# Optimization experiments

Hardware: AMD Instinct MI355X
Metric: run time of the kernel (lower is better)

The kernel has to match this reference:

```python
import jax, jax.numpy as jnp
import numpy as np

DIM = 1024
NUM_HEAD = 16
N_IMG = 64


def _linear_params(key, scale=0.02):
    kw, kb = jax.random.split(key)
    W = jax.random.normal(kw, (DIM, DIM), jnp.float32) * scale
    b = jax.random.normal(kb, (DIM,), jnp.float32) * scale
    return W, b


def setup_inputs() -> dict:
    key = jax.random.key(0)
    ks = jax.random.split(key, 5)
    # ragged per-image instance counts: 128..254, deterministic, sum = 12224
    lens = (128 + 2 * np.arange(N_IMG)).astype(np.int64)
    N = int(lens.sum())  # 12224
    x = jax.random.normal(ks[0], (N, DIM), jnp.float32)
    Wq, bq = _linear_params(ks[1])
    Wk, bk = _linear_params(ks[2])
    Wv, bv = _linear_params(ks[3])
    Wu, bu = _linear_params(ks[4])
    return {"x": x, "Wq": Wq, "bq": bq, "Wk": Wk, "bk": bk,
            "Wv": Wv, "bv": bv, "Wu": Wu, "bu": bu,
            "num_inst_per_image": jnp.asarray(lens)}


def _segment_layout(num_inst_per_image):
    # static (int) metadata -> numpy; returns padded gather idx, key mask, unpad idx
    lens = np.asarray(num_inst_per_image)
    B = lens.shape[0]
    L = int(lens.max())
    offsets = np.concatenate([[0], np.cumsum(lens)[:-1]])
    pos = offsets[:, None] + np.arange(L)[None, :]           # [B, L] flat positions
    valid = np.arange(L)[None, :] < lens[:, None]            # [B, L]
    gather_idx = jnp.asarray(np.where(valid, pos, 0))        # safe gather
    flat_take = jnp.asarray(np.flatnonzero(valid.ravel()))   # [N] unpad (row-major = segment order)
    return gather_idx, jnp.asarray(valid), flat_take, B, L


def reference(x, Wq, bq, Wk, bk, Wv, bv, Wu, bu, num_inst_per_image):
    gather_idx, valid, flat_take, B, L = _segment_layout(num_inst_per_image)
    N, C = x.shape
    H = NUM_HEAD
    D = C // H
    # global QKV projections on the flat batch (as in the torch module)
    q = (x @ Wq + bq)[gather_idx].reshape(B, L, H, D)
    k = (x @ Wk + bk)[gather_idx].reshape(B, L, H, D)
    v = (x @ Wv + bv)[gather_idx].reshape(B, L, H, D)
    scale = 1.0 / np.sqrt(C)  # note: original divides by sqrt(C), not sqrt(head_dim)
    attn = jnp.einsum('bqhd,bkhd->bhqk', q, k) * scale       # [B, H, L, L]
    bias = jnp.where(valid[:, None, None, :], 0.0, -jnp.inf)  # mask padded keys
    attn = jax.nn.softmax(attn + bias, axis=-1)
    out = jnp.einsum('bhqk,bkhd->bqhd', attn, v).reshape(B * L, C)
    out = out[flat_take]                                      # unpad back to [N, C]
    return out @ Wu + bu
```

## Files before the change

### kernel.cpp

```cpp
#include <hip/hip_runtime.h>
#include <hip/hip_bf16.h>
#include <math.h>

#define DIMC 1024
#define NHEAD 16
#define HDIM 64
#define MPAD 12288

using bf16x8 = __attribute__((ext_vector_type(8))) short;
using f32x4  = __attribute__((ext_vector_type(4))) float;
using f32x16 = __attribute__((ext_vector_type(16))) float;

__device__ inline ushort f2bf(float f) {
    uint u = __float_as_uint(f);
    u += 0x7fffu + ((u >> 16) & 1u);
    return (ushort)(u >> 16);
}
__device__ inline float bf2f(ushort h) { return __uint_as_float(((uint)h) << 16); }

__device__ inline uint pkbf(float a, float b) {
    __hip_bfloat162 t = __float22bfloat162_rn(float2{a, b});
    return *reinterpret_cast<uint*>(&t);
}

__device__ inline void gload_lds16(const ushort* g, ushort* l) {
    __builtin_amdgcn_global_load_lds(
        (const __attribute__((address_space(1))) uint*)g,
        (__attribute__((address_space(3))) uint*)l, 16, 0, 0);
}

__global__ __launch_bounds__(256) void gemm_qkv(
    const ushort* __restrict__ A, const ushort* __restrict__ Bt,
    const float* __restrict__ bq, const float* __restrict__ bk,
    const float* __restrict__ bv,
    ushort* __restrict__ qb, ushort* __restrict__ kb, ushort* __restrict__ vb,
    int M)
{
    __shared__ ushort As[128 * 32];
    __shared__ ushort Bs[128 * 32];

    const int bid = blockIdx.x;
    const int xcd = bid & 7;
    const int j   = bid >> 3;
    const int mt  = xcd * 12 + (j % 12);
    const int nt  = j / 12;
    const int row0 = mt * 128, col0 = nt * 128;

    const int t    = threadIdx.x;
    const int w    = t >> 6;
    const int lane = t & 63;
    const int wr   = (w >> 1) * 64;
    const int wc   = (w & 1) * 64;
    const int frow = lane & 15;
    const int fk   = (lane >> 4) * 8;
    const int arow = lane >> 2;
    const int acol = (lane & 3) * 8;

    f32x4 acc[4][4] = {};

    for (int k0 = 0; k0 < DIMC; k0 += 32) {
        #pragma unroll
        for (int i = 0; i < 2; ++i) {
            const int rr = (i * 4 + w) * 16;
            gload_lds16(A  + (size_t)(row0 + rr + arow) * DIMC + k0 + acol, As + rr * 32);
            gload_lds16(Bt + (size_t)(col0 + rr + arow) * DIMC + k0 + acol, Bs + rr * 32);
        }
        __syncthreads();

        bf16x8 af[4], bfr[4];
        #pragma unroll
        for (int m = 0; m < 4; ++m)
            af[m]  = *(const bf16x8*)&As[(wr + m * 16 + frow) * 32 + fk];
        #pragma unroll
        for (int n = 0; n < 4; ++n)
            bfr[n] = *(const bf16x8*)&Bs[(wc + n * 16 + frow) * 32 + fk];

        #pragma unroll
        for (int m = 0; m < 4; ++m)
            #pragma unroll
            for (int n = 0; n < 4; ++n)
                acc[m][n] = __builtin_amdgcn_mfma_f32_16x16x32_bf16(
                    af[m], bfr[n], acc[m][n], 0, 0, 0);
        __syncthreads();
    }

    const int sel = nt >> 3;
    const float* bias = (sel == 0) ? bq : (sel == 1) ? bk : bv;
    ushort* outp      = (sel == 0) ? qb : (sel == 1) ? kb : vb;
    const int colb = col0 - sel * 1024;

    const int r4 = (lane >> 4) * 4;
    #pragma unroll
    for (int n = 0; n < 4; ++n) {
        const int c  = colb + wc + n * 16 + (lane & 15);
        const float bb = bias[c];
        #pragma unroll
        for (int m = 0; m < 4; ++m) {
            #pragma unroll
            for (int r = 0; r < 4; ++r) {
                const int gr = row0 + wr + m * 16 + r4 + r;
                if (gr < M)
                    outp[(size_t)gr * DIMC + c] = f2bf(acc[m][n][r] + bb);
            }
        }
    }
}

__global__ __launch_bounds__(256) void gemm_final(
    const ushort* __restrict__ A, const ushort* __restrict__ Bt,
    const float* __restrict__ bias, float* __restrict__ C, int M)
{
    __shared__ ushort As[128 * 32];
    __shared__ ushort Bs[128 * 32];

    const int bid = blockIdx.x;
    const int xcd = bid & 7;
    const int j   = bid >> 3;
    const int mt  = xcd * 12 + (j % 12);
    const int nt  = j / 12;
    const int row0 = mt * 128, col0 = nt * 128;

    const int t    = threadIdx.x;
    const int w    = t >> 6;
    const int lane = t & 63;
    const int wr   = (w >> 1) * 64;
    const int wc   = (w & 1) * 64;
    const int frow = lane & 15;
    const int fk   = (lane >> 4) * 8;
    const int arow = lane >> 2;
    const int acol = (lane & 3) * 8;

    f32x4 acc[4][4] = {};

    for (int k0 = 0; k0 < DIMC; k0 += 32) {
        #pragma unroll
        for (int i = 0; i < 2; ++i) {
            const int rr = (i * 4 + w) * 16;
            gload_lds16(A  + (size_t)(row0 + rr + arow) * DIMC + k0 + acol, As + rr * 32);
            gload_lds16(Bt + (size_t)(col0 + rr + arow) * DIMC + k0 + acol, Bs + rr * 32);
        }
        __syncthreads();

        bf16x8 af[4], bfr[4];
        #pragma unroll
        for (int m = 0; m < 4; ++m)
            af[m]  = *(const bf16x8*)&As[(wr + m * 16 + frow) * 32 + fk];
        #pragma unroll
        for (int n = 0; n < 4; ++n)
            bfr[n] = *(const bf16x8*)&Bs[(wc + n * 16 + frow) * 32 + fk];

        #pragma unroll
        for (int m = 0; m < 4; ++m)
            #pragma unroll
            for (int n = 0; n < 4; ++n)
                acc[m][n] = __builtin_amdgcn_mfma_f32_16x16x32_bf16(
                    af[m], bfr[n], acc[m][n], 0, 0, 0);
        __syncthreads();
    }

    const int r4 = (lane >> 4) * 4;
    #pragma unroll
    for (int n = 0; n < 4; ++n) {
        const int c  = col0 + wc + n * 16 + (lane & 15);
        const float bb = bias[c];
        #pragma unroll
        for (int m = 0; m < 4; ++m) {
            #pragma unroll
            for (int r = 0; r < 4; ++r) {
                const int gr = row0 + wr + m * 16 + r4 + r;
                if (gr < M)
                    C[(size_t)gr * DIMC + c] = acc[m][n][r] + bb;
            }
        }
    }
}

__global__ __launch_bounds__(256) void cvt_pad(
    const float* __restrict__ x, ushort* __restrict__ xb, int nvalid, int ntot)
{
    const int stride = gridDim.x * blockDim.x;
    for (int i = blockIdx.x * blockDim.x + threadIdx.x; i < ntot / 4; i += stride) {
        const int e = i * 4;
        ushort4 o;
        if (e < nvalid) {
            const float4 f = *(const float4*)(x + e);
            o.x = f2bf(f.x); o.y = f2bf(f.y); o.z = f2bf(f.z); o.w = f2bf(f.w);
        } else { o.x = o.y = o.z = o.w = 0; }
        *(ushort4*)(xb + e) = o;
    }
}

__global__ __launch_bounds__(256) void transpose_w4(
    const float* __restrict__ W0, const float* __restrict__ W1,
    const float* __restrict__ W2, const float* __restrict__ W3,
    ushort* __restrict__ T0, ushort* __restrict__ T1,
    ushort* __restrict__ T2, ushort* __restrict__ T3)
{
    __shared__ float tile[32][33];
    const int z = blockIdx.z;
    const float* W = (z == 0) ? W0 : (z == 1) ? W1 : (z == 2) ? W2 : W3;
    ushort*      T = (z == 0) ? T0 : (z == 1) ? T1 : (z == 2) ? T2 : T3;
    const int tx = threadIdx.x & 31;
    const int ty = threadIdx.x >> 5;
    const int n0 = blockIdx.x * 32;
    const int k0 = blockIdx.y * 32;
    #pragma unroll
    for (int i = 0; i < 32; i += 8)
        tile[ty + i][tx] = W[(size_t)(k0 + ty + i) * DIMC + n0 + tx];
    __syncthreads();
    #pragma unroll
    for (int i = 0; i < 32; i += 8)
        T[(size_t)(n0 + ty + i) * DIMC + k0 + tx] = f2bf(tile[tx][ty + i]);
}

__global__ __launch_bounds__(64) void attn_mfma(
    const ushort* __restrict__ qg, const ushort* __restrict__ kg,
    const ushort* __restrict__ vg, ushort* __restrict__ og,
    const int* __restrict__ lens, int B)
{
    __shared__ ushort Vt[64 * 68];

    const int i   = blockIdx.x;
    const int xcd = i & 7;
    const int j   = i >> 3;
    const int bh  = xcd * (B * 2) + (j >> 2);
    const int qt  = j & 3;
    const int h   = bh & 15;
    const int b   = bh >> 4;

    const int lane = threadIdx.x & 63;

    const int myl = (lane < B) ? lens[lane] : 0;
    int inc = myl;
    #pragma unroll
    for (int d = 1; d < 64; d <<= 1) {
        const int nb = __shfl_up(inc, d);
        if (lane >= d) inc += nb;
    }
    const int off = __shfl(inc, b) - __shfl(myl, b);
    const int L   = __shfl(myl, b);
    if (qt * 64 >= L) return;
    const int ntk = (L + 63) >> 6;

    const int l31 = lane & 31;
    const int hi  = lane >> 5;
    const int kp  = lane & 31;
    const int dh  = lane >> 5;

    bf16x8 qf[2][4];
    #pragma unroll
    for (int qn = 0; qn < 2; ++qn) {
        const size_t row = (size_t)(off + min(qt * 64 + qn * 32 + l31, L - 1));
        #pragma unroll
        for (int ks = 0; ks < 4; ++ks) {
            union { uint4 u4; ushort us[8]; bf16x8 v; } tmp;
            tmp.u4 = *(const uint4*)(qg + row * DIMC + h * HDIM + ks * 16 + hi * 8);
            #pragma unroll
            for (int e = 0; e < 8; ++e)
                tmp.us[e] = f2bf(bf2f(tmp.us[e]) * 0.03125f);
            qf[qn][ks] = tmp.v;
        }
    }

    f32x16 o[2][2] = {};
    float mst[2] = {-1e30f, -1e30f};
    float lst[2] = {0.f, 0.f};

    uint4 va[4], vbr[4];
    auto issueV = [&](int tt) {
        const int j0s = tt * 64;
        #pragma unroll
        for (int it = 0; it < 4; ++it) {
            const int d0 = (it * 2 + dh) * 8;
            const size_t r0 = (size_t)(off + min(j0s + 2 * kp,     L - 1));
            const size_t r1 = (size_t)(off + min(j0s + 2 * kp + 1, L - 1));
            va[it]  = *(const uint4*)(vg + r0 * DIMC + h * HDIM + d0);
            vbr[it] = *(const uint4*)(vg + r1 * DIMC + h * HDIM + d0);
        }
    };

    bf16x8 kfc[2][4], kfn[2][4];
    auto loadK = [&](int tt, bf16x8 (&kf)[2][4]) {
        const int j0s = tt * 64;
        #pragma unroll
        for (int km = 0; km < 2; ++km) {
            const size_t row = (size_t)(off + min(j0s + km * 32 + l31, L - 1));
            #pragma unroll
            for (int ks = 0; ks < 4; ++ks)
                kf[km][ks] = *(const bf16x8*)(kg + row * DIMC + h * HDIM + ks * 16 + hi * 8);
        }
    };

    issueV(0);
    loadK(0, kfc);

    for (int t = 0; t < ntk; ++t) {
        const int j0 = t * 64;

        loadK(min(t + 1, ntk - 1), kfn);

        f32x16 s[2][2] = {};
        __builtin_amdgcn_s_setprio(1);
        #pragma unroll
        for (int km = 0; km < 2; ++km)
            #pragma unroll
            for (int qn = 0; qn < 2; ++qn)
                #pragma unroll
                for (int ks = 0; ks < 4; ++ks)
                    s[km][qn] = __builtin_amdgcn_mfma_f32_32x32x16_bf16(
                        kfc[km][ks], qf[qn][ks], s[km][qn], 0, 0, 0);
        __builtin_amdgcn_s_setprio(0);

        #pragma unroll
        for (int it = 0; it < 4; ++it) {
            const int d0 = (it * 2 + dh) * 8;
            const uint a4[4] = {va[it].x,  va[it].y,  va[it].z,  va[it].w};
            const uint b4[4] = {vbr[it].x, vbr[it].y, vbr[it].z, vbr[it].w};
            #pragma unroll
            for (int jj = 0; jj < 4; ++jj) {
                const uint lo  = (a4[jj] & 0xffffu) | (b4[jj] << 16);
                const uint hi2 = (a4[jj] >> 16) | (b4[jj] & 0xffff0000u);
                *(uint*)&Vt[(d0 + 2 * jj)     * 68 + 2 * kp] = lo;
                *(uint*)&Vt[(d0 + 2 * jj + 1) * 68 + 2 * kp] = hi2;
            }
        }
        if (t + 1 < ntk) issueV(t + 1);

        const bool fullTile = (j0 + 64 <= L);
        float tmv[2];
        #pragma unroll
        for (int qn = 0; qn < 2; ++qn) {
            float tm = -1e30f;
            if (fullTile) {
                #pragma unroll
                for (int km = 0; km < 2; ++km)
                    #pragma unroll
                    for (int r = 0; r < 16; ++r)
                        tm = fmaxf(tm, s[km][qn][r]);
            } else {
                #pragma unroll
                for (int km = 0; km < 2; ++km)
                    #pragma unroll
                    for (int r = 0; r < 16; ++r) {
                        const int key = j0 + km * 32 + (r & 3) + 8 * (r >> 2) + 4 * hi;
                        float sv = s[km][qn][r];
                        sv = (key < L) ? sv : -1e30f;
                        s[km][qn][r] = sv;
                        tm = fmaxf(tm, sv);
                    }
            }
            tm = fmaxf(tm, __shfl_xor(tm, 32));
            tmv[qn] = tm;
        }

        const bool need = (tmv[0] > mst[0] + 4.f) || (tmv[1] > mst[1] + 4.f);
        if (__any(need)) {
            #pragma unroll
            for (int qn = 0; qn < 2; ++qn) {
                const float nm = fmaxf(mst[qn], tmv[qn]);
                const float corr = __expf(mst[qn] - nm);
                mst[qn] = nm;
                lst[qn] *= corr;
                #pragma unroll
                for (int dm = 0; dm < 2; ++dm)
                    #pragma unroll
                    for (int r = 0; r < 16; ++r)
                        o[dm][qn][r] *= corr;
            }
        }
        #pragma unroll
        for (int qn = 0; qn < 2; ++qn) {
            float ls = 0.f;
            #pragma unroll
            for (int km = 0; km < 2; ++km)
                #pragma unroll
                for (int r = 0; r < 16; ++r) {
                    const float p = __expf(s[km][qn][r] - mst[qn]);
                    s[km][qn][r] = p;
                    ls += p;
                }
            ls += __shfl_xor(ls, 32);
            lst[qn] += ls;
        }

        #pragma unroll
        for (int kspv = 0; kspv < 4; ++kspv) {
            const int km = kspv >> 1;
            const int sb = kspv & 1;

            bf16x8 Afr[2];
            #pragma unroll
            for (int dm = 0; dm < 2; ++dm) {
                const int d = dm * 32 + l31;
                const uint2 p0 = *(const uint2*)&Vt[d * 68 + kspv * 16 + hi * 8];
                const uint2 p1 = *(const uint2*)&Vt[d * 68 + kspv * 16 + hi * 8 + 4];
                union { uint u[4]; bf16x8 v; } aa;
                aa.u[0] = p0.x; aa.u[1] = p0.y; aa.u[2] = p1.x; aa.u[3] = p1.y;
                Afr[dm] = aa.v;
            }

            bf16x8 Bfr[2];
            #pragma unroll
            for (int qn = 0; qn < 2; ++qn) {
                const uint X0 = pkbf(s[km][qn][8 * sb + 0], s[km][qn][8 * sb + 1]);
                const uint X1 = pkbf(s[km][qn][8 * sb + 2], s[km][qn][8 * sb + 3]);
                const uint Y0 = pkbf(s[km][qn][8 * sb + 4], s[km][qn][8 * sb + 5]);
                const uint Y1 = pkbf(s[km][qn][8 * sb + 6], s[km][qn][8 * sb + 7]);
                const uint sx0 = (uint)__shfl_xor((int)X0, 32);
                const uint sx1 = (uint)__shfl_xor((int)X1, 32);
                const uint sy0 = (uint)__shfl_xor((int)Y0, 32);
                const uint sy1 = (uint)__shfl_xor((int)Y1, 32);
                union { uint u[4]; bf16x8 v; } bb;
                bb.u[0] = hi ? sy0 : X0;
                bb.u[1] = hi ? sy1 : X1;
                bb.u[2] = hi ? Y0 : sx0;
                bb.u[3] = hi ? Y1 : sx1;
                Bfr[qn] = bb.v;
            }

            __builtin_amdgcn_s_setprio(1);
            #pragma unroll
            for (int dm = 0; dm < 2; ++dm)
                #pragma unroll
                for (int qn = 0; qn < 2; ++qn)
                    o[dm][qn] = __builtin_amdgcn_mfma_f32_32x32x16_bf16(
                        Afr[dm], Bfr[qn], o[dm][qn], 0, 0, 0);
            __builtin_amdgcn_s_setprio(0);
        }

        #pragma unroll
        for (int km = 0; km < 2; ++km)
            #pragma unroll
            for (int ks = 0; ks < 4; ++ks)
                kfc[km][ks] = kfn[km][ks];
    }

    #pragma unroll
    for (int qn = 0; qn < 2; ++qn) {
        const int q = qt * 64 + qn * 32 + l31;
        if (q < L) {
            const float inv = 1.f / lst[qn];
            ushort* orow = og + (size_t)(off + q) * DIMC + h * HDIM;
            #pragma unroll
            for (int dm = 0; dm < 2; ++dm)
                #pragma unroll
                for (int bq2 = 0; bq2 < 4; ++bq2) {
                    const int r0 = 4 * bq2;
                    uint2 st;
                    st.x = pkbf(o[dm][qn][r0 + 0] * inv, o[dm][qn][r0 + 1] * inv);
                    st.y = pkbf(o[dm][qn][r0 + 2] * inv, o[dm][qn][r0 + 3] * inv);
                    *(uint2*)(orow + dm * 32 + 8 * bq2 + 4 * hi) = st;
                }
        }
    }
}

extern "C" void kernel_launch(void* const* d_in, const int* in_sizes, int n_in,
                              void* d_out, int out_size, void* d_ws, size_t ws_size,
                              hipStream_t stream)
{
    const float* x   = (const float*)d_in[0];
    const float* Wq  = (const float*)d_in[1];
    const float* bq  = (const float*)d_in[2];
    const float* Wk  = (const float*)d_in[3];
    const float* bk  = (const float*)d_in[4];
    const float* Wv  = (const float*)d_in[5];
    const float* bv  = (const float*)d_in[6];
    const float* Wu  = (const float*)d_in[7];
    const float* bu  = (const float*)d_in[8];
    const int*  lens = (const int*)d_in[9];

    const int N = in_sizes[0] / DIMC;
    const int B = in_sizes[9];

    ushort* xb  = (ushort*)d_ws;
    ushort* wtq = xb  + (size_t)MPAD * DIMC;
    ushort* wtk = wtq + (size_t)DIMC * DIMC;
    ushort* wtv = wtk + (size_t)DIMC * DIMC;
    ushort* wtu = wtv + (size_t)DIMC * DIMC;
    ushort* kb  = wtu + (size_t)DIMC * DIMC;
    ushort* vb  = kb  + (size_t)N * DIMC;
    ushort* qb  = (ushort*)d_out;
    ushort* ob  = xb;

    cvt_pad<<<2048, 256, 0, stream>>>(x, xb, N * DIMC, MPAD * DIMC);
    transpose_w4<<<dim3(32, 32, 4), 256, 0, stream>>>(Wq, Wk, Wv, Wu,
                                                      wtq, wtk, wtv, wtu);

    gemm_qkv<<<2304, 256, 0, stream>>>(xb, wtq, bq, bk, bv, qb, kb, vb, N);

    attn_mfma<<<dim3(B * NHEAD * 4), dim3(64), 0, stream>>>(qb, kb, vb, ob, lens, B);

    gemm_final<<<768, 256, 0, stream>>>(ob, wtu, bu, (float*)d_out, N);
}
```

Measured before the change: 241.5 us.

## Replace 128x128 GEMMs with 256x256 double-buffered swizzled-LDS GEMM template

```diff
diff --git a/kernel.cpp b/kernel.cpp
--- a/kernel.cpp
+++ b/kernel.cpp
@@ -29,147 +29,169 @@
         (__attribute__((address_space(3))) uint*)l, 16, 0, 0);
 }
 
-__global__ __launch_bounds__(256) void gemm_qkv(
+template <bool BF16OUT>
+__global__ __launch_bounds__(512, 2) void gemm256(
     const ushort* __restrict__ A, const ushort* __restrict__ Bt,
-    const float* __restrict__ bq, const float* __restrict__ bk,
-    const float* __restrict__ bv,
-    ushort* __restrict__ qb, ushort* __restrict__ kb, ushort* __restrict__ vb,
-    int M)
+    const float* __restrict__ bias0, const float* __restrict__ bias1,
+    const float* __restrict__ bias2,
+    void* __restrict__ out0, void* __restrict__ out1, void* __restrict__ out2,
+    int M, int mtPerXcd, int mtTotal)
 {
-    __shared__ ushort As[128 * 32];
-    __shared__ ushort Bs[128 * 32];
+    __shared__ ushort lds[2][2][256 * 64];
 
     const int bid = blockIdx.x;
     const int xcd = bid & 7;
     const int j   = bid >> 3;
-    const int mt  = xcd * 12 + (j % 12);
-    const int nt  = j / 12;
-    const int row0 = mt * 128, col0 = nt * 128;
-
-    const int t    = threadIdx.x;
-    const int w    = t >> 6;
-    const int lane = t & 63;
-    const int wr   = (w >> 1) * 64;
-    const int wc   = (w & 1) * 64;
-    const int frow = lane & 15;
-    const int fk   = (lane >> 4) * 8;
-    const int arow = lane >> 2;
-    const int acol = (lane & 3) * 8;
-
-    f32x4 acc[4][4] = {};
-
-    for (int k0 = 0; k0 < DIMC; k0 += 32) {
-        #pragma unroll
-        for (int i = 0; i < 2; ++i) {
-            const int rr = (i * 4 + w) * 16;
-            gload_lds16(A  + (size_t)(row0 + rr + arow) * DIMC + k0 + acol, As + rr * 32);
-            gload_lds16(Bt + (size_t)(col0 + rr + arow) * DIMC + k0 + acol, Bs + rr * 32);
-        }
-        __syncthreads();
-
-        bf16x8 af[4], bfr[4];
-        #pragma unroll
-        for (int m = 0; m < 4; ++m)
-            af[m]  = *(const bf16x8*)&As[(wr + m * 16 + frow) * 32 + fk];
-        #pragma unroll
-        for (int n = 0; n < 4; ++n)
-            bfr[n] = *(const bf16x8*)&Bs[(wc + n * 16 + frow) * 32 + fk];
-
-        #pragma unroll
-        for (int m = 0; m < 4; ++m)
-            #pragma unroll
-            for (int n = 0; n < 4; ++n)
-                acc[m][n] = __builtin_amdgcn_mfma_f32_16x16x32_bf16(
-                    af[m], bfr[n], acc[m][n], 0, 0, 0);
-        __syncthreads();
-    }
-
-    const int sel = nt >> 3;
-    const float* bias = (sel == 0) ? bq : (sel == 1) ? bk : bv;
-    ushort* outp      = (sel == 0) ? qb : (sel == 1) ? kb : vb;
-    const int colb = col0 - sel * 1024;
-
-    const int r4 = (lane >> 4) * 4;
+    const int mt  = xcd * mtPerXcd + (j % mtPerXcd);
+    const int nt  = j / mtPerXcd;
+    const int row0 = mt * 256;
+    const int col0 = nt * 256;
+
+    const int t512 = threadIdx.x;
+    const int w    = t512 >> 6;
+    const int lane = t512 & 63;
+    const int wm   = w >> 2;
+    const int wn   = w & 3;
+    const int l15  = lane & 15;
+    const int kh   = lane >> 4;
+
+    auto stage = [&](int buf, int kt, int mat, int relRow) {
+        const int o   = relRow * 128 + lane * 16;
+        const int row = o >> 7;
+        const int kb  = (o & 127) ^ ((row & 7) << 4);
+        const ushort* src = (mat ? Bt + (size_t)(col0 + row) * DIMC
+                                 : A  + (size_t)(row0 + row) * DIMC)
+                            + kt * 64 + (kb >> 1);
+        gload_lds16(src, &lds[buf][mat][0] + relRow * 64);
+    };
+
+    auto rdA = [&](int buf, int qr, int fr, int ks) -> bf16x8 {
+        const int row = wm * 128 + qr * 64 + fr * 16 + l15;
+        const int ad  = (row * 128 + ks * 64 + kh * 16) ^ ((row & 7) << 4);
+        return *(const bf16x8*)(&lds[buf][0][0] + (ad >> 1));
+    };
+    auto rdB = [&](int buf, int qc, int fc, int ks) -> bf16x8 {
+        const int row = wn * 64 + qc * 32 + fc * 16 + l15;
+        const int ad  = (row * 128 + ks * 64 + kh * 16) ^ ((row & 7) << 4);
+        return *(const bf16x8*)(&lds[buf][1][0] + (ad >> 1));
+    };
+
+    f32x4 acc[8][4] = {};
+    bf16x8 af[4][2];
+    bf16x8 bq[2][2][2];
+
+    stage(0, 0, 0, wm * 128 + wn * 16);
+    stage(0, 0, 0, wm * 128 + wn * 16 + 8);
+    stage(0, 0, 1, wn * 64 + wm * 16);
+    stage(0, 0, 1, wn * 64 + wm * 16 + 8);
+    stage(0, 0, 1, wn * 64 + 32 + wm * 16);
+    stage(0, 0, 1, wn * 64 + 32 + wm * 16 + 8);
+    stage(0, 0, 0, wm * 128 + 64 + wn * 16);
+    stage(0, 0, 0, wm * 128 + 64 + wn * 16 + 8);
+
+    const int NT = DIMC / 64;
+    for (int t = 0; t < NT; ++t) {
+        const int cur = t & 1;
+        const int nxt = cur ^ 1;
+        const int tn  = (t + 1 < NT) ? (t + 1) : (NT - 1);
+
+        asm volatile("s_waitcnt vmcnt(4)" ::: "memory");
+        __builtin_amdgcn_s_barrier();
+        __builtin_amdgcn_sched_barrier(0);
+        #pragma unroll
+        for (int fr = 0; fr < 4; ++fr)
+            #pragma unroll
+            for (int ks = 0; ks < 2; ++ks)
+                af[fr][ks] = rdA(cur, 0, fr, ks);
+        #pragma unroll
+        for (int fc = 0; fc < 2; ++fc)
+            #pragma unroll
+            for (int ks = 0; ks < 2; ++ks)
+                bq[0][fc][ks] = rdB(cur, 0, fc, ks);
+        stage(nxt, tn, 0, wm * 128 + wn * 16);
+        stage(nxt, tn, 0, wm * 128 + wn * 16 + 8);
+        stage(nxt, tn, 1, wn * 64 + wm * 16);
+        stage(nxt, tn, 1, wn * 64 + wm * 16 + 8);
+        __builtin_amdgcn_s_setprio(1);
+        #pragma unroll
+        for (int fr = 0; fr < 4; ++fr)
+            #pragma unroll
+            for (int fc = 0; fc < 2; ++fc)
+                #pragma unroll
+                for (int ks = 0; ks < 2; ++ks)
+                    acc[fr][fc] = __builtin_amdgcn_mfma_f32_16x16x32_bf16(
+                        af[fr][ks], bq[0][fc][ks], acc[fr][fc], 0, 0, 0);
+        __builtin_amdgcn_s_setprio(0);
+
+        asm volatile("s_waitcnt vmcnt(6)" ::: "memory");
+        __builtin_amdgcn_s_barrier();
+        __builtin_amdgcn_sched_barrier(0);
+        #pragma unroll
+        for (int fc = 0; fc < 2; ++fc)
+            #pragma unroll
+            for (int ks = 0; ks < 2; ++ks)
+                bq[1][fc][ks] = rdB(cur, 1, fc, ks);
+        stage(nxt, tn, 1, wn * 64 + 32 + wm * 16);
+        stage(nxt, tn, 1, wn * 64 + 32 + wm * 16 + 8);
+        __builtin_amdgcn_s_setprio(1);
+        #pragma unroll
+        for (int fr = 0; fr < 4; ++fr)
+            #pragma unroll
+            for (int fc = 0; fc < 2; ++fc)
+                #pragma unroll
+                for (int ks = 0; ks < 2; ++ks)
+                    acc[fr][2 + fc] = __builtin_amdgcn_mfma_f32_16x16x32_bf16(
+                        af[fr][ks], bq[1][fc][ks], acc[fr][2 + fc], 0, 0, 0);
+        __builtin_amdgcn_s_setprio(0);
+
+        asm volatile("s_waitcnt vmcnt(6)" ::: "memory");
+        __builtin_amdgcn_s_barrier();
+        __builtin_amdgcn_sched_barrier(0);
+        #pragma unroll
+        for (int fr = 0; fr < 4; ++fr)
+            #pragma unroll
+            for (int ks = 0; ks < 2; ++ks)
+                af[fr][ks] = rdA(cur, 1, fr, ks);
+        stage(nxt, tn, 0, wm * 128 + 64 + wn * 16);
+        stage(nxt, tn, 0, wm * 128 + 64 + wn * 16 + 8);
+        __builtin_amdgcn_s_setprio(1);
+        #pragma unroll
+        for (int fr = 0; fr < 4; ++fr)
+            #pragma unroll
+            for (int fc = 0; fc < 2; ++fc)
+                #pragma unroll
+                for (int ks = 0; ks < 2; ++ks)
+                    acc[4 + fr][fc] = __builtin_amdgcn_mfma_f32_16x16x32_bf16(
+                        af[fr][ks], bq[0][fc][ks], acc[4 + fr][fc], 0, 0, 0);
+        #pragma unroll
+        for (int fr = 0; fr < 4; ++fr)
+            #pragma unroll
+            for (int fc = 0; fc < 2; ++fc)
+                #pragma unroll
+                for (int ks = 0; ks < 2; ++ks)
+                    acc[4 + fr][2 + fc] = __builtin_amdgcn_mfma_f32_16x16x32_bf16(
+                        af[fr][ks], bq[1][fc][ks], acc[4 + fr][2 + fc], 0, 0, 0);
+        __builtin_amdgcn_s_setprio(0);
+    }
+
+    const int sel  = nt >> 2;
+    const float* bias = (sel == 0) ? bias0 : (sel == 1) ? bias1 : bias2;
+    void* outp        = (sel == 0) ? out0  : (sel == 1) ? out1  : out2;
+    const int r4 = kh * 4;
     #pragma unroll
     for (int n = 0; n < 4; ++n) {
-        const int c  = colb + wc + n * 16 + (lane & 15);
+        const int c  = (nt & 3) * 256 + wn * 64 + n * 16 + l15;
         const float bb = bias[c];
         #pragma unroll
-        for (int m = 0; m < 4; ++m) {
+        for (int i = 0; i < 8; ++i) {
             #pragma unroll
             for (int r = 0; r < 4; ++r) {
-                const int gr = row0 + wr + m * 16 + r4 + r;
-                if (gr < M)
-                    outp[(size_t)gr * DIMC + c] = f2bf(acc[m][n][r] + bb);
-            }
-        }
-    }
-}
-
-__global__ __launch_bounds__(256) void gemm_final(
-    const ushort* __restrict__ A, const ushort* __restrict__ Bt,
-    const float* __restrict__ bias, float* __restrict__ C, int M)
-{
-    __shared__ ushort As[128 * 32];
-    __shared__ ushort Bs[128 * 32];
-
-    const int bid = blockIdx.x;
-    const int xcd = bid & 7;
-    const int j   = bid >> 3;
-    const int mt  = xcd * 12 + (j % 12);
-    const int nt  = j / 12;
-    const int row0 = mt * 128, col0 = nt * 128;
-
-    const int t    = threadIdx.x;
-    const int w    = t >> 6;
-    const int lane = t & 63;
-    const int wr   = (w >> 1) * 64;
-    const int wc   = (w & 1) * 64;
-    const int frow = lane & 15;
-    const int fk   = (lane >> 4) * 8;
-    const int arow = lane >> 2;
-    const int acol = (lane & 3) * 8;
-
-    f32x4 acc[4][4] = {};
-
-    for (int k0 = 0; k0 < DIMC; k0 += 32) {
-        #pragma unroll
-        for (int i = 0; i < 2; ++i) {
-            const int rr = (i * 4 + w) * 16;
-            gload_lds16(A  + (size_t)(row0 + rr + arow) * DIMC + k0 + acol, As + rr * 32);
-            gload_lds16(Bt + (size_t)(col0 + rr + arow) * DIMC + k0 + acol, Bs + rr * 32);
-        }
-        __syncthreads();
-
-        bf16x8 af[4], bfr[4];
-        #pragma unroll
-        for (int m = 0; m < 4; ++m)
-            af[m]  = *(const bf16x8*)&As[(wr + m * 16 + frow) * 32 + fk];
-        #pragma unroll
-        for (int n = 0; n < 4; ++n)
-            bfr[n] = *(const bf16x8*)&Bs[(wc + n * 16 + frow) * 32 + fk];
-
-        #pragma unroll
-        for (int m = 0; m < 4; ++m)
-            #pragma unroll
-            for (int n = 0; n < 4; ++n)
-                acc[m][n] = __builtin_amdgcn_mfma_f32_16x16x32_bf16(
-                    af[m], bfr[n], acc[m][n], 0, 0, 0);
-        __syncthreads();
-    }
-
-    const int r4 = (lane >> 4) * 4;
-    #pragma unroll
-    for (int n = 0; n < 4; ++n) {
-        const int c  = col0 + wc + n * 16 + (lane & 15);
-        const float bb = bias[c];
-        #pragma unroll
-        for (int m = 0; m < 4; ++m) {
-            #pragma unroll
-            for (int r = 0; r < 4; ++r) {
-                const int gr = row0 + wr + m * 16 + r4 + r;
-                if (gr < M)
-                    C[(size_t)gr * DIMC + c] = acc[m][n][r] + bb;
+                const int gr = row0 + wm * 128 + i * 16 + r4 + r;
+                if (gr < M) {
+                    const float val = acc[i][n][r] + bb;
+                    if (BF16OUT) ((ushort*)outp)[(size_t)gr * DIMC + c] = f2bf(val);
+                    else         ((float*)outp)[(size_t)gr * DIMC + c]  = val;
+                }
             }
         }
     }
@@ -487,9 +509,11 @@
     transpose_w4<<<dim3(32, 32, 4), 256, 0, stream>>>(Wq, Wk, Wv, Wu,
                                                       wtq, wtk, wtv, wtu);
 
-    gemm_qkv<<<2304, 256, 0, stream>>>(xb, wtq, bq, bk, bv, qb, kb, vb, N);
+    gemm256<true><<<576, 512, 0, stream>>>(xb, wtq, bq, bk, bv,
+                                           qb, kb, vb, N, 6, 48);
 
     attn_mfma<<<dim3(B * NHEAD * 4), dim3(64), 0, stream>>>(qb, kb, vb, ob, lens, B);
 
-    gemm_final<<<768, 256, 0, stream>>>(ob, wtu, bu, (float*)d_out, N);
-}
+    gemm256<false><<<192, 512, 0, stream>>>(ob, wtu, bu, bu, bu,
+                                            d_out, d_out, d_out, N, 6, 48);
+}
```

Result: slower. 253.0 us (+4.8%).
